# Kernel tuning notes

Measured on AMD Instinct MI355X. Metric: run time of the kernel, lower is better.

The kernel has to match this reference:

```python
import jax, jax.numpy as jnp
import numpy as np

HIDDEN = 50


def _lstm_layer(x_tbi, w_ih, w_hh, b_ih, b_hh):
    """One LSTM layer, PyTorch gate order (i, f, g, o).
    x_tbi: [T, B, in]; returns h sequence [T, B, H]."""
    B = x_tbi.shape[1]
    H = w_hh.shape[1]
    # Precompute input projections for all timesteps at once (one big GEMM).
    x_proj = jnp.einsum('tbi,gi->tbg', x_tbi, w_ih) + b_ih + b_hh  # [T, B, 4H]

    def step(carry, xp):
        h, c = carry
        gates = xp + h @ w_hh.T  # [B, 4H]
        i, f, g, o = jnp.split(gates, 4, axis=-1)
        i = jax.nn.sigmoid(i)
        f = jax.nn.sigmoid(f)
        g = jnp.tanh(g)
        o = jax.nn.sigmoid(o)
        c = f * c + i * g
        h = o * jnp.tanh(c)
        return (h, c), h

    h0 = jnp.zeros((B, H), dtype=x_tbi.dtype)
    c0 = jnp.zeros((B, H), dtype=x_tbi.dtype)
    _, hs = jax.lax.scan(step, (h0, c0), x_proj)
    return hs  # [T, B, H]


def setup_inputs() -> dict:
    key = jax.random.key(0)
    ks = jax.random.split(key, 12)
    B, T, I, H = 2048, 512, 12, HIDDEN
    s_in = 1.0 / np.sqrt(H)  # PyTorch LSTM init scale
    inp = {
        'x': jax.random.normal(ks[0], (B, T, I), dtype=jnp.float32),
        'w_ih0': jax.random.uniform(ks[1], (4 * H, I), jnp.float32, -s_in, s_in),
        'w_hh0': jax.random.uniform(ks[2], (4 * H, H), jnp.float32, -s_in, s_in),
        'b_ih0': jax.random.uniform(ks[3], (4 * H,), jnp.float32, -s_in, s_in),
        'b_hh0': jax.random.uniform(ks[4], (4 * H,), jnp.float32, -s_in, s_in),
        'w_ih1': jax.random.uniform(ks[5], (4 * H, H), jnp.float32, -s_in, s_in),
        'w_hh1': jax.random.uniform(ks[6], (4 * H, H), jnp.float32, -s_in, s_in),
        'b_ih1': jax.random.uniform(ks[7], (4 * H,), jnp.float32, -s_in, s_in),
        'b_hh1': jax.random.uniform(ks[8], (4 * H,), jnp.float32, -s_in, s_in),
        'w_out': jax.random.uniform(ks[9], (1, H), jnp.float32, -s_in, s_in),
        'b_out': jax.random.uniform(ks[10], (1,), jnp.float32, -s_in, s_in),
    }
    return inp


def reference(x, w_ih0, w_hh0, b_ih0, b_hh0, w_ih1, w_hh1, b_ih1, b_hh1, w_out, b_out):
    # x: [B, T, I] (batch_first). Scan works over leading time axis.
    x_tbi = jnp.transpose(x, (1, 0, 2))  # [T, B, I]
    h1 = _lstm_layer(x_tbi, w_ih0, w_hh0, b_ih0, b_hh0)  # [T, B, H]
    h2 = _lstm_layer(h1, w_ih1, w_hh1, b_ih1, b_hh1)     # [T, B, H]
    last = h2[-1]                                         # r_out[:, -1, :] -> [B, H]
    logits = last @ w_out.T + b_out                       # [B, 1]
    return jax.nn.sigmoid(logits)
```

## Files before the change

kernel.cpp:

```cpp
#include <hip/hip_runtime.h>

#define TT   512
#define BI   12
#define HH   50
#define BB   8
#define BTOT 2048
#define LOG2E 1.4426950408889634f


typedef _Float16 half8 __attribute__((ext_vector_type(8)));
typedef float    f4    __attribute__((ext_vector_type(4)));

__device__ __forceinline__ float sigm_(float v) {
    return __builtin_amdgcn_rcpf(1.f + __builtin_amdgcn_exp2f(v * (-LOG2E)));
}
__device__ __forceinline__ float dppmerge_(float a0, float a1) {
    int r = __builtin_amdgcn_update_dpp(__builtin_bit_cast(int, a0),
                                        __builtin_bit_cast(int, a1),
                                        0x128, 0xF, 0xC, false);
    return __builtin_bit_cast(float, r);
}

__launch_bounds__(1024)
__global__ void lstm2_kernel(const float* __restrict__ x,
                             const float* __restrict__ w_ih0, const float* __restrict__ w_hh0,
                             const float* __restrict__ b_ih0, const float* __restrict__ b_hh0,
                             const float* __restrict__ w_ih1, const float* __restrict__ w_hh1,
                             const float* __restrict__ b_ih1, const float* __restrict__ b_hh1,
                             const float* __restrict__ w_out, const float* __restrict__ b_out,
                             float* __restrict__ out)
{
    const int tid   = threadIdx.x;
    const int wv    = tid >> 6;
    const int lane  = tid & 63;
    const int layer = wv >> 3;
    const int w8    = wv & 7;
    const int b0    = blockIdx.x * BB;
    const int t0     = (w8 < 5) ? 2 * w8 : (5 + w8);
    const int ntiles = (w8 < 5) ? 2 : 1;

    if (layer) __builtin_amdgcn_s_setprio(1);

    __shared__ __align__(16) _Float16 B0s[2][64 * 16];
    __shared__ __align__(16) _Float16 B1s[2][64 * 16];

    const int m = lane & 15;
    const int q = lane >> 4;
    half8 af[2][4];
    #pragma unroll
    for (int s = 0; s < 2; s++) {
        #pragma unroll
        for (int kb = 0; kb < 4; kb++) {
            #pragma unroll
            for (int j = 0; j < 8; j++) {
                float v = 0.f;
                if (s < ntiles && (layer == 1 || kb < 2)) {
                    const int T  = t0 + s;
                    const int u  = T * 4 + (m >> 2);
                    const int g  = m & 3;
                    const int kg = kb * 32 + q * 8 + j;
                    if (u < HH) {
                        const int r = g * HH + u;
                        if (layer == 0) {
                            if      (kg < 50)  v = w_hh0[r * HH + kg];
                            else if (kg < 62)  v = w_ih0[r * BI + (kg - 50)];
                            else if (kg == 62) v = b_ih0[r] + b_hh0[r];
                        } else {
                            if      (kg < 50)               v = w_ih1[r * HH + kg];
                            else if (kg >= 64 && kg < 114)  v = w_hh1[r * HH + (kg - 64)];
                            else if (kg == 126)             v = b_ih1[r] + b_hh1[r];
                        }
                        v *= (g == 2) ? (2.f * LOG2E) : (-LOG2E);
                    }
                }
                af[s][kb][j] = (_Float16)v;
            }
        }
    }

    for (int i = tid; i < 2 * 64 * 16; i += 1024) {
        (&B0s[0][0])[i] = (_Float16)0.f;
        (&B1s[0][0])[i] = (_Float16)0.f;
    }
    __syncthreads();
    if (tid < 16) {
        B0s[0][7 * 128 + tid * 8 + 6] = (_Float16)1.f;
        B0s[1][7 * 128 + tid * 8 + 6] = (_Float16)1.f;
        B1s[0][7 * 128 + tid * 8 + 6] = (_Float16)1.f;
        B1s[1][7 * 128 + tid * 8 + 6] = (_Float16)1.f;
    }

    const int n16  = lane & 15;
    const int slot = n16 >> 3;
    const int bcol = n16 & 7;
    const int u_m  = (t0 + slot) * 4 + q;
    const bool wvalid = (u_m < HH) && (slot == 0 || ntiles == 2);
    float cm = 0.f;

    const bool xact = (layer == 0) && (ntiles == 1) && (slot == 1);
    const int xidx  = (w8 - 5) * 32 + q * 8 + bcol;
    const int xb    = xidx / 12, xi = xidx - xb * 12;
    const int xrow  = 50 + xi;
    const int xoff  = (xrow >> 3) * 128 + xb * 8 + (xrow & 7);
    const size_t xbase = ((size_t)(b0 + xb) * TT) * BI + xi;
    if (xact)
        B0s[0][xoff] = (_Float16)x[xbase];
    __syncthreads();

    const _Float16* rd0[2] = { &B0s[0][0] + lane * 8, &B0s[1][0] + lane * 8 };
    const _Float16* rd1[2] = { &B1s[0][0] + lane * 8, &B1s[1][0] + lane * 8 };
    const int offA = (u_m >> 3) * 128 + bcol * 8 + (u_m & 7);
    _Float16* wAp[2] = { (layer ? &B1s[0][0] : &B0s[0][0]) + offA,
                         (layer ? &B1s[1][0] : &B0s[1][0]) + offA };
    _Float16* xdp[2] = { &B0s[0][0] + xoff, &B0s[1][0] + xoff };

    const f4 fzero = {0.f, 0.f, 0.f, 0.f};

    const float* xq = x + xbase + BI;
    float xhold = 0.f;
    if (xact) xhold = *xq;
    xq += BI;

#define STEP(P, DOL0, DOL1, DOST, DOLD)                                       \
  {                                                                           \
    float xnew = 0.f;                                                         \
    if ((DOLD) && xact) xnew = *xq;                                           \
    if ((DOST) && xact) *xdp[1 - (P)] = (_Float16)xhold;                      \
    if ((layer == 0) ? (DOL0) : (DOL1)) {                                     \
      const half8 bf0 = *(const half8*)(rd0[P]);                              \
      const half8 bf1 = *(const half8*)(rd0[P] + 512);                        \
      f4 acc0, acc1 = fzero;                                                  \
      if (layer == 0) {                                                       \
        acc0 = __builtin_amdgcn_mfma_f32_16x16x32_f16(af[0][0], bf0, fzero, 0, 0, 0); \
        acc0 = __builtin_amdgcn_mfma_f32_16x16x32_f16(af[0][1], bf1, acc0, 0, 0, 0);  \
        if (ntiles > 1) {                                                     \
          acc1 = __builtin_amdgcn_mfma_f32_16x16x32_f16(af[1][0], bf0, fzero, 0, 0, 0); \
          acc1 = __builtin_amdgcn_mfma_f32_16x16x32_f16(af[1][1], bf1, acc1, 0, 0, 0);  \
        }                                                                     \
      } else {                                                                \
        const half8 bf2 = *(const half8*)(rd1[P]);                            \
        const half8 bf3 = *(const half8*)(rd1[P] + 512);                      \
        acc0 = __builtin_amdgcn_mfma_f32_16x16x32_f16(af[0][0], bf0, fzero, 0, 0, 0); \
        acc0 = __builtin_amdgcn_mfma_f32_16x16x32_f16(af[0][1], bf1, acc0, 0, 0, 0);  \
        acc0 = __builtin_amdgcn_mfma_f32_16x16x32_f16(af[0][2], bf2, acc0, 0, 0, 0);  \
        acc0 = __builtin_amdgcn_mfma_f32_16x16x32_f16(af[0][3], bf3, acc0, 0, 0, 0);  \
        if (ntiles > 1) {                                                     \
          acc1 = __builtin_amdgcn_mfma_f32_16x16x32_f16(af[1][0], bf0, fzero, 0, 0, 0); \
          acc1 = __builtin_amdgcn_mfma_f32_16x16x32_f16(af[1][1], bf1, acc1, 0, 0, 0);  \
          acc1 = __builtin_amdgcn_mfma_f32_16x16x32_f16(af[1][2], bf2, acc1, 0, 0, 0);  \
          acc1 = __builtin_amdgcn_mfma_f32_16x16x32_f16(af[1][3], bf3, acc1, 0, 0, 0);  \
        }                                                                     \
      }                                                                       \
      f4 am;                                                                  \
      _Pragma("unroll")                                                       \
      for (int i = 0; i < 4; i++) am[i] = dppmerge_(acc0[i], acc1[i]);        \
      const float eI = __builtin_amdgcn_exp2f(am[0]);                         \
      const float eF = __builtin_amdgcn_exp2f(am[1]);                         \
      const float eG = __builtin_amdgcn_exp2f(am[2]);                         \
      const float eO = __builtin_amdgcn_exp2f(am[3]);                         \
      const float dI = 1.f + eI, dF = 1.f + eF;                               \
      const float dG = 1.f + eG, dO = 1.f + eO;                               \
      const float pIG = dI * dG;                                              \
      const float num = __builtin_fmaf(cm, pIG, (eG - 1.f) * dF);             \
      cm = num * __builtin_amdgcn_rcpf(dF * pIG);                             \
      const float uu = fminf(cm * (2.f * LOG2E), 60.f);                       \
      const float eC = __builtin_amdgcn_exp2f(uu);                            \
      const float h  = (eC - 1.f) * __builtin_amdgcn_rcpf(dO * (1.f + eC));   \
      if (wvalid) *wAp[1 - (P)] = (_Float16)h;                                \
    }                                                                         \
    if (DOLD) { xhold = xnew; xq += BI; }                                     \
    __syncthreads();                                                          \
  }

    STEP(0, 1, 0, 1, 1)
    STEP(1, 1, 1, 1, 1)
    #pragma unroll 1
    for (int it = 0; it < 254; ++it) {
        STEP(0, 1, 1, 1, 1)
        STEP(1, 1, 1, 1, 1)
    }
    STEP(0, 1, 1, 1, 0)
    STEP(1, 1, 1, 0, 0)
    STEP(0, 0, 1, 0, 0)
#undef STEP

    if (tid < BB) {
        float s = b_out[0];
        #pragma unroll
        for (int u = 0; u < HH; u++) {
            s += w_out[u] * (float)B1s[1][(u >> 3) * 128 + tid * 8 + (u & 7)];
        }
        out[b0 + tid] = sigm_(s);
    }
}

extern "C" void kernel_launch(void* const* d_in, const int* in_sizes, int n_in,
                              void* d_out, int out_size, void* d_ws, size_t ws_size,
                              hipStream_t stream) {
    const float* x     = (const float*)d_in[0];
    const float* w_ih0 = (const float*)d_in[1];
    const float* w_hh0 = (const float*)d_in[2];
    const float* b_ih0 = (const float*)d_in[3];
    const float* b_hh0 = (const float*)d_in[4];
    const float* w_ih1 = (const float*)d_in[5];
    const float* w_hh1 = (const float*)d_in[6];
    const float* b_ih1 = (const float*)d_in[7];
    const float* b_hh1 = (const float*)d_in[8];
    const float* w_out = (const float*)d_in[9];
    const float* b_out = (const float*)d_in[10];
    float* out = (float*)d_out;

    dim3 grid(BTOT / BB);
    dim3 block(1024);
    lstm2_kernel<<<grid, block, 0, stream>>>(x, w_ih0, w_hh0, b_ih0, b_hh0,
                                             w_ih1, w_hh1, b_ih1, b_hh1,
                                             w_out, b_out, out);
}
```

Measured before the change: 355.3 us.

## Assign each gate tile to one wave computing both layers via DPP merge

```diff
diff --git a/kernel.cpp b/kernel.cpp
--- a/kernel.cpp
+++ b/kernel.cpp
@@ -33,48 +33,55 @@
     const int tid   = threadIdx.x;
     const int wv    = tid >> 6;
     const int lane  = tid & 63;
-    const int layer = wv >> 3;
-    const int w8    = wv & 7;
     const int b0    = blockIdx.x * BB;
-    const int t0     = (w8 < 5) ? 2 * w8 : (5 + w8);
-    const int ntiles = (w8 < 5) ? 2 : 1;
-
-    if (layer) __builtin_amdgcn_s_setprio(1);
+
+    const int m    = lane & 15;
+    const int q    = lane >> 4;
+    const int slot = m >> 3;
+    const int bcol = m & 7;
+    const int T    = wv;
+    const bool comp = (wv < 13);
+    const int u_m  = T * 4 + q;
+    const bool wvalid = comp && (u_m < HH);
+
+    if (comp) __builtin_amdgcn_s_setprio(1);
 
     __shared__ __align__(16) _Float16 B0s[2][64 * 16];
     __shared__ __align__(16) _Float16 B1s[2][64 * 16];
 
-    const int m = lane & 15;
-    const int q = lane >> 4;
-    half8 af[2][4];
+    const int uA = T * 4 + (m >> 2);
+    const int gA = m & 3;
+    half8 af0[2], af1[4];
     #pragma unroll
-    for (int s = 0; s < 2; s++) {
+    for (int kb = 0; kb < 2; kb++) {
         #pragma unroll
-        for (int kb = 0; kb < 4; kb++) {
-            #pragma unroll
-            for (int j = 0; j < 8; j++) {
-                float v = 0.f;
-                if (s < ntiles && (layer == 1 || kb < 2)) {
-                    const int T  = t0 + s;
-                    const int u  = T * 4 + (m >> 2);
-                    const int g  = m & 3;
-                    const int kg = kb * 32 + q * 8 + j;
-                    if (u < HH) {
-                        const int r = g * HH + u;
-                        if (layer == 0) {
-                            if      (kg < 50)  v = w_hh0[r * HH + kg];
-                            else if (kg < 62)  v = w_ih0[r * BI + (kg - 50)];
-                            else if (kg == 62) v = b_ih0[r] + b_hh0[r];
-                        } else {
-                            if      (kg < 50)               v = w_ih1[r * HH + kg];
-                            else if (kg >= 64 && kg < 114)  v = w_hh1[r * HH + (kg - 64)];
-                            else if (kg == 126)             v = b_ih1[r] + b_hh1[r];
-                        }
-                        v *= (g == 2) ? (2.f * LOG2E) : (-LOG2E);
-                    }
-                }
-                af[s][kb][j] = (_Float16)v;
+        for (int j = 0; j < 8; j++) {
+            float v = 0.f;
+            if (comp && uA < HH) {
+                const int r  = gA * HH + uA;
+                const int kg = kb * 32 + q * 8 + j;
+                if      (kg < 50)  v = w_hh0[r * HH + kg];
+                else if (kg < 62)  v = w_ih0[r * BI + (kg - 50)];
+                else if (kg == 62) v = b_ih0[r] + b_hh0[r];
+                v *= (gA == 2) ? (2.f * LOG2E) : (-LOG2E);
             }
+            af0[kb][j] = (_Float16)v;
+        }
+    }
+    #pragma unroll
+    for (int kb = 0; kb < 4; kb++) {
+        #pragma unroll
+        for (int j = 0; j < 8; j++) {
+            float v = 0.f;
+            if (comp && uA < HH) {
+                const int r  = gA * HH + uA;
+                const int kg = kb * 32 + q * 8 + j;
+                if      (kg < 50)               v = w_ih1[r * HH + kg];
+                else if (kg >= 64 && kg < 114)  v = w_hh1[r * HH + (kg - 64)];
+                else if (kg == 126)             v = b_ih1[r] + b_hh1[r];
+                v *= (gA == 2) ? (2.f * LOG2E) : (-LOG2E);
+            }
+            af1[kb][j] = (_Float16)v;
         }
     }
 
@@ -90,15 +97,8 @@
         B1s[1][7 * 128 + tid * 8 + 6] = (_Float16)1.f;
     }
 
-    const int n16  = lane & 15;
-    const int slot = n16 >> 3;
-    const int bcol = n16 & 7;
-    const int u_m  = (t0 + slot) * 4 + q;
-    const bool wvalid = (u_m < HH) && (slot == 0 || ntiles == 2);
-    float cm = 0.f;
-
-    const bool xact = (layer == 0) && (ntiles == 1) && (slot == 1);
-    const int xidx  = (w8 - 5) * 32 + q * 8 + bcol;
+    const bool xact = (wv >= 13) && (lane < 32);
+    const int xidx  = (wv - 13) * 32 + lane;
     const int xb    = xidx / 12, xi = xidx - xb * 12;
     const int xrow  = 50 + xi;
     const int xoff  = (xrow >> 3) * 128 + xb * 8 + (xrow & 7);
@@ -110,11 +110,12 @@
     const _Float16* rd0[2] = { &B0s[0][0] + lane * 8, &B0s[1][0] + lane * 8 };
     const _Float16* rd1[2] = { &B1s[0][0] + lane * 8, &B1s[1][0] + lane * 8 };
     const int offA = (u_m >> 3) * 128 + bcol * 8 + (u_m & 7);
-    _Float16* wAp[2] = { (layer ? &B1s[0][0] : &B0s[0][0]) + offA,
-                         (layer ? &B1s[1][0] : &B0s[1][0]) + offA };
+    _Float16* wAp[2] = { (slot ? &B1s[0][0] : &B0s[0][0]) + offA,
+                         (slot ? &B1s[1][0] : &B0s[1][0]) + offA };
     _Float16* xdp[2] = { &B0s[0][0] + xoff, &B0s[1][0] + xoff };
 
     const f4 fzero = {0.f, 0.f, 0.f, 0.f};
+    float cm = 0.f;
 
     const float* xq = x + xbase + BI;
     float xhold = 0.f;
@@ -126,31 +127,18 @@
     float xnew = 0.f;                                                         \
     if ((DOLD) && xact) xnew = *xq;                                           \
     if ((DOST) && xact) *xdp[1 - (P)] = (_Float16)xhold;                      \
-    if ((layer == 0) ? (DOL0) : (DOL1)) {                                     \
+    if (comp) {                                                               \
       const half8 bf0 = *(const half8*)(rd0[P]);                              \
       const half8 bf1 = *(const half8*)(rd0[P] + 512);                        \
-      f4 acc0, acc1 = fzero;                                                  \
-      if (layer == 0) {                                                       \
-        acc0 = __builtin_amdgcn_mfma_f32_16x16x32_f16(af[0][0], bf0, fzero, 0, 0, 0); \
-        acc0 = __builtin_amdgcn_mfma_f32_16x16x32_f16(af[0][1], bf1, acc0, 0, 0, 0);  \
-        if (ntiles > 1) {                                                     \
-          acc1 = __builtin_amdgcn_mfma_f32_16x16x32_f16(af[1][0], bf0, fzero, 0, 0, 0); \
-          acc1 = __builtin_amdgcn_mfma_f32_16x16x32_f16(af[1][1], bf1, acc1, 0, 0, 0);  \
-        }                                                                     \
-      } else {                                                                \
-        const half8 bf2 = *(const half8*)(rd1[P]);                            \
-        const half8 bf3 = *(const half8*)(rd1[P] + 512);                      \
-        acc0 = __builtin_amdgcn_mfma_f32_16x16x32_f16(af[0][0], bf0, fzero, 0, 0, 0); \
-        acc0 = __builtin_amdgcn_mfma_f32_16x16x32_f16(af[0][1], bf1, acc0, 0, 0, 0);  \
-        acc0 = __builtin_amdgcn_mfma_f32_16x16x32_f16(af[0][2], bf2, acc0, 0, 0, 0);  \
-        acc0 = __builtin_amdgcn_mfma_f32_16x16x32_f16(af[0][3], bf3, acc0, 0, 0, 0);  \
-        if (ntiles > 1) {                                                     \
-          acc1 = __builtin_amdgcn_mfma_f32_16x16x32_f16(af[1][0], bf0, fzero, 0, 0, 0); \
-          acc1 = __builtin_amdgcn_mfma_f32_16x16x32_f16(af[1][1], bf1, acc1, 0, 0, 0);  \
-          acc1 = __builtin_amdgcn_mfma_f32_16x16x32_f16(af[1][2], bf2, acc1, 0, 0, 0);  \
-          acc1 = __builtin_amdgcn_mfma_f32_16x16x32_f16(af[1][3], bf3, acc1, 0, 0, 0);  \
-        }                                                                     \
-      }                                                                       \
+      const half8 bf2 = *(const half8*)(rd1[P]);                              \
+      const half8 bf3 = *(const half8*)(rd1[P] + 512);                        \
+      f4 acc0, acc1;                                                          \
+      acc0 = __builtin_amdgcn_mfma_f32_16x16x32_f16(af0[0], bf0, fzero, 0, 0, 0); \
+      acc0 = __builtin_amdgcn_mfma_f32_16x16x32_f16(af0[1], bf1, acc0, 0, 0, 0);  \
+      acc1 = __builtin_amdgcn_mfma_f32_16x16x32_f16(af1[0], bf0, fzero, 0, 0, 0); \
+      acc1 = __builtin_amdgcn_mfma_f32_16x16x32_f16(af1[1], bf1, acc1, 0, 0, 0);  \
+      acc1 = __builtin_amdgcn_mfma_f32_16x16x32_f16(af1[2], bf2, acc1, 0, 0, 0);  \
+      acc1 = __builtin_amdgcn_mfma_f32_16x16x32_f16(af1[3], bf3, acc1, 0, 0, 0);  \
       f4 am;                                                                  \
       _Pragma("unroll")                                                       \
       for (int i = 0; i < 4; i++) am[i] = dppmerge_(acc0[i], acc1[i]);        \
@@ -162,11 +150,13 @@
       const float dG = 1.f + eG, dO = 1.f + eO;                               \
       const float pIG = dI * dG;                                              \
       const float num = __builtin_fmaf(cm, pIG, (eG - 1.f) * dF);             \
-      cm = num * __builtin_amdgcn_rcpf(dF * pIG);                             \
-      const float uu = fminf(cm * (2.f * LOG2E), 60.f);                       \
-      const float eC = __builtin_amdgcn_exp2f(uu);                            \
-      const float h  = (eC - 1.f) * __builtin_amdgcn_rcpf(dO * (1.f + eC));   \
-      if (wvalid) *wAp[1 - (P)] = (_Float16)h;                                \
+      const float cmn = num * __builtin_amdgcn_rcpf(dF * pIG);                \
+      const float uu  = fminf(cmn * (2.f * LOG2E), 60.f);                     \
+      const float eC  = __builtin_amdgcn_exp2f(uu);                           \
+      const float h   = (eC - 1.f) * __builtin_amdgcn_rcpf(dO * (1.f + eC));  \
+      const bool actp = slot ? (bool)(DOL1) : (bool)(DOL0);                   \
+      if (actp) cm = cmn;                                                     \
+      if (actp && wvalid) *wAp[1 - (P)] = (_Float16)h;                        \
     }                                                                         \
     if (DOLD) { xhold = xnew; xq += BI; }                                     \
     __syncthreads();                                                          \
```

Result: no change. 350.0 us (-1.5%).
